# Optimization experiments

Measured on AMD Instinct MI355X. Metric: run time of the kernel, lower is better.

The kernel has to match this reference:

```python
import jax, jax.numpy as jnp
import numpy as np

N, DIN, C, E = 50000, 256, 8, 1600000
N_STEPS = 5


def setup_inputs() -> dict:
    key = jax.random.key(0)
    k1, k2, k3, k4 = jax.random.split(key, 4)
    x = jax.random.normal(k1, (N, DIN), dtype=jnp.float32)
    W = jax.random.normal(k2, (DIN, C), dtype=jnp.float32) / np.float32(np.sqrt(DIN))
    b = jnp.zeros((C,), dtype=jnp.float32)
    edge_index = jax.random.randint(k3, (2, E), 0, N, dtype=jnp.int64)
    rv = jax.random.randint(k4, (E,), 0, E, dtype=jnp.int64)
    return {"x": x, "W": W, "b": b, "edge_index": edge_index, "rv": rv}


def _log_normalize(lx):
    return lx - jax.scipy.special.logsumexp(lx, axis=-1, keepdims=True)


def reference(x, W, b, edge_index, rv):
    # transform: Linear (num_hidden=0) + LogSoftmax -> initial log beliefs
    log_b0 = jax.nn.log_softmax(x @ W + b, axis=-1)            # [N, C]
    src, dst = edge_index[0], edge_index[1]
    n_nodes, n_cls = log_b0.shape
    # learn_coupling=False: log_H = -3 * (ones - eye)
    logH = -3.0 * (jnp.ones((n_cls, n_cls), jnp.float32) - jnp.eye(n_cls, dtype=jnp.float32))
    log_msg = jnp.full((edge_index.shape[1], n_cls), -np.log(n_cls), dtype=jnp.float32)
    log_b = log_b0
    for _ in range(N_STEPS):
        x_j = log_b[src]                                        # [E, C] gather
        t = x_j - log_msg[rv]                                   # [E, C]
        # per-edge logsumexp over incoming class dim against coupling matrix
        raw = jax.scipy.special.logsumexp(t[:, :, None] + logH[None, :, :], axis=1)  # [E, C]
        log_msg = _log_normalize(raw)
        agg = jax.ops.segment_sum(log_msg, dst, num_segments=n_nodes)  # scatter-add
        log_b = _log_normalize(agg + log_b0)
    return log_b
```

## Files before the change

kernel.cpp:

```cpp
#include <hip/hip_runtime.h>

static constexpr int kN   = 50000;
static constexpr int kDin = 256;
static constexpr int kC   = 8;
static constexpr int kE   = 1600000;
static constexpr int kSteps = 5;

static constexpr int kNB      = 256;
static constexpr int kBucketW = 196;
static constexpr int kChunk   = 4096;
static constexpr int kEperB   = kE / kNB;

static constexpr size_t OFF_LOGB0 = 0;
static constexpr size_t OFF_BHIST = 1600000;
static constexpr size_t OFF_GBASE = 1601024;
static constexpr size_t OFF_GCUR  = 1602112;
static constexpr size_t OFF_START = 1603200;
static constexpr size_t OFF_REC   = 1803264;
static constexpr size_t OFF_PAY   = 8203264;
static constexpr size_t OFF_INV   = 21003264;
static constexpr size_t OFF_MSGA  = 27403264;
static constexpr size_t OFF_MSGB  = 40203264;
static constexpr size_t OFF_SPOS  = 53003264;
static constexpr size_t OFF_SRCS  = 59403264;
static constexpr size_t OFF_RVT   = 62603264;
static constexpr size_t OFF_RVS   = 69003264;
static constexpr size_t OFF_REC2  = 75403264;
static constexpr size_t OFF_GCUR2 = 88203264;
static constexpr size_t WS_NEEDED = 88204288;

static constexpr float kDEC8  = 3.0f / 255.0f;
static constexpr float kENC8  = 255.0f / 3.0f;
static constexpr float kOFF   = 3.2990003f;
static constexpr float kA     = 0.049787068367863944f;
static constexpr float kOneMA = 0.950212931632136f;

__global__ void __launch_bounds__(256) init_kernel(
    const float* __restrict__ x, const float* __restrict__ W,
    const float* __restrict__ bias,
    float* __restrict__ log_b0, float* __restrict__ log_b,
    const int* __restrict__ dst, int* __restrict__ bhist)
{
    __shared__ int h[kNB];
    if (blockIdx.x >= 1024) {
        h[threadIdx.x] = 0;
        __syncthreads();
        const int nthr = 256 * 256;
        for (int e = (blockIdx.x - 1024) * 256 + threadIdx.x; e < kE; e += nthr)
            atomicAdd(&h[dst[e] / kBucketW], 1);
        __syncthreads();
        if (h[threadIdx.x]) atomicAdd(&bhist[threadIdx.x], h[threadIdx.x]);
        return;
    }

    const int lane   = threadIdx.x & 63;
    const int wave   = (blockIdx.x * 256 + threadIdx.x) >> 6;
    const int nwaves = (1024 * 256) >> 6;

    float w[4][8];
#pragma unroll
    for (int j = 0; j < 4; ++j) {
        const float4* wp = reinterpret_cast<const float4*>(W + (size_t)(lane + 64 * j) * kC);
        float4 a = wp[0], b2 = wp[1];
        w[j][0] = a.x;  w[j][1] = a.y;  w[j][2] = a.z;  w[j][3] = a.w;
        w[j][4] = b2.x; w[j][5] = b2.y; w[j][6] = b2.z; w[j][7] = b2.w;
    }

    for (int row = wave; row < kN; row += nwaves) {
        const float* xr = x + (size_t)row * kDin;
        float acc[8] = {0.f, 0.f, 0.f, 0.f, 0.f, 0.f, 0.f, 0.f};
#pragma unroll
        for (int j = 0; j < 4; ++j) {
            float xv = xr[lane + 64 * j];
#pragma unroll
            for (int c = 0; c < 8; ++c) acc[c] = fmaf(xv, w[j][c], acc[c]);
        }
#pragma unroll
        for (int off = 32; off > 0; off >>= 1) {
#pragma unroll
            for (int c = 0; c < 8; ++c) acc[c] += __shfl_down(acc[c], off, 64);
        }
        if (lane == 0) {
            float z[8], m = -1e30f;
#pragma unroll
            for (int c = 0; c < 8; ++c) { z[c] = acc[c] + bias[c]; m = fmaxf(m, z[c]); }
            float s = 0.f;
#pragma unroll
            for (int c = 0; c < 8; ++c) s += __expf(z[c] - m);
            float lse = m + __logf(s);
#pragma unroll
            for (int c = 0; c < 8; ++c) {
                float v = z[c] - lse;
                log_b0[(size_t)row * 8 + c] = v;
                log_b[(size_t)row * 8 + c]  = v;
            }
        }
    }
}

__global__ void __launch_bounds__(256) bucket_scan_kernel(
    const int* __restrict__ bhist, int* __restrict__ gbase, int* __restrict__ gcur,
    int* __restrict__ gcur2)
{
    __shared__ int sh[kNB];
    const int tid = threadIdx.x;
    int v = bhist[tid];
    sh[tid] = v;
    __syncthreads();
#pragma unroll
    for (int off = 1; off < kNB; off <<= 1) {
        int t = (tid >= off) ? sh[tid - off] : 0;
        __syncthreads();
        sh[tid] += t;
        __syncthreads();
    }
    int excl = sh[tid] - v;
    gbase[tid] = excl;
    gcur[tid]  = excl;
    gcur2[tid] = tid * kEperB;
    if (tid == kNB - 1) { gbase[kNB] = sh[tid]; gcur[kNB] = sh[tid]; }
}

__global__ void __launch_bounds__(256) bin_kernel(
    const int* __restrict__ dst, const int* __restrict__ src,
    const int* __restrict__ rv, int* __restrict__ gcur,
    unsigned int* __restrict__ recbuf, unsigned long long* __restrict__ paybuf)
{
    __shared__ int hist[kNB];
    __shared__ int sh[kNB];
    __shared__ int cursor[kNB];
    __shared__ int gdbase[kNB];
    __shared__ unsigned int buf[kChunk];
    __shared__ unsigned long long pbuf[kChunk];

    const int tid = threadIdx.x;
    const int e0  = blockIdx.x * kChunk;
    const int n   = (kE - e0 < kChunk) ? (kE - e0) : kChunk;

    hist[tid] = 0;
    __syncthreads();

    int myb[16];
    unsigned int rec[16];
    unsigned long long pay[16];
#pragma unroll
    for (int k = 0; k < 16; ++k) {
        const int i = tid + k * 256;
        myb[k] = -1;
        if (i < n) {
            const int d = dst[e0 + i];
            const int b = d / kBucketW;
            myb[k] = b;
            rec[k] = ((unsigned int)(d - b * kBucketW) << 21) | (unsigned int)(e0 + i);
            pay[k] = ((unsigned long long)(unsigned int)src[e0 + i] << 21)
                   | (unsigned int)rv[e0 + i];
            atomicAdd(&hist[b], 1);
        }
    }
    __syncthreads();

    const int cnt = hist[tid];
    sh[tid] = cnt;
    __syncthreads();
#pragma unroll
    for (int off = 1; off < kNB; off <<= 1) {
        int t = (tid >= off) ? sh[tid - off] : 0;
        __syncthreads();
        sh[tid] += t;
        __syncthreads();
    }
    const int excl = sh[tid] - cnt;
    cursor[tid] = excl;
    __syncthreads();

#pragma unroll
    for (int k = 0; k < 16; ++k) {
        if (myb[k] >= 0) {
            int slot = atomicAdd(&cursor[myb[k]], 1);
            buf[slot]  = rec[k];
            pbuf[slot] = pay[k];
        }
    }
    gdbase[tid] = (cnt > 0) ? atomicAdd(&gcur[tid], cnt) : 0;
    __syncthreads();

    for (int i = tid; i < n; i += 256) {
        int b = 0;
#pragma unroll
        for (int step = 128; step >= 1; step >>= 1)
            if (b + step <= kNB - 1 && sh[b + step - 1] <= i) b += step;
        const int off_in_b = i - (sh[b] - hist[b]);
        recbuf[gdbase[b] + off_in_b] = buf[i];
        paybuf[gdbase[b] + off_in_b] = pbuf[i];
    }
}

__global__ void __launch_bounds__(256) fine_kernel(
    const int* __restrict__ gbase, const unsigned int* __restrict__ recbuf,
    const unsigned long long* __restrict__ paybuf,
    int* __restrict__ start, int* __restrict__ inv,
    unsigned short* __restrict__ src_s, int* __restrict__ rvt)
{
    __shared__ int hist[kNB];
    __shared__ int sh[kNB];
    __shared__ int lcur[kNB];

    const int tid = threadIdx.x;
    const int b   = blockIdx.x;
    const int nb0 = b * kBucketW;
    const int nnode = (kN - nb0 < kBucketW) ? (kN - nb0) : kBucketW;
    const int rb = gbase[b], re = gbase[b + 1];

    hist[tid] = 0;
    __syncthreads();

    for (int i = rb + tid; i < re; i += 256)
        atomicAdd(&hist[recbuf[i] >> 21], 1);
    __syncthreads();

    const int cnt = hist[tid];
    sh[tid] = cnt;
    __syncthreads();
#pragma unroll
    for (int off = 1; off < kNB; off <<= 1) {
        int t = (tid >= off) ? sh[tid - off] : 0;
        __syncthreads();
        sh[tid] += t;
        __syncthreads();
    }
    const int excl = sh[tid] - cnt;
    lcur[tid] = rb + excl;
    if (tid < nnode) start[nb0 + tid] = rb + excl;
    if (b == gridDim.x - 1 && tid == 0) start[kN] = kE;
    __syncthreads();

    for (int i = rb + tid; i < re; i += 256) {
        const unsigned int r = recbuf[i];
        const unsigned long long pay = paybuf[i];
        const int p = atomicAdd(&lcur[r >> 21], 1);
        inv[p]   = (int)(r & 0x1FFFFFu);
        src_s[p] = (unsigned short)(pay >> 21);
        rvt[p]   = (int)(pay & 0x1FFFFFu);
    }
}

__global__ void __launch_bounds__(256) bin2_kernel(
    const int* __restrict__ inv, int* __restrict__ gcur2,
    unsigned long long* __restrict__ recbuf2)
{
    __shared__ int hist[kNB];
    __shared__ int sh[kNB];
    __shared__ int cursor[kNB];
    __shared__ int gdbase[kNB];
    __shared__ unsigned long long buf[kChunk];

    const int tid = threadIdx.x;
    const int p0  = blockIdx.x * kChunk;
    const int n   = (kE - p0 < kChunk) ? (kE - p0) : kChunk;

    hist[tid] = 0;
    __syncthreads();

    int myb[16];
    unsigned long long rec[16];
#pragma unroll
    for (int k = 0; k < 16; ++k) {
        const int i = tid + k * 256;
        myb[k] = -1;
        if (i < n) {
            const int e = inv[p0 + i];
            const int b = e / kEperB;
            myb[k] = b;
            rec[k] = ((unsigned long long)(e - b * kEperB) << 32) | (unsigned int)(p0 + i);
            atomicAdd(&hist[b], 1);
        }
    }
    __syncthreads();

    const int cnt = hist[tid];
    sh[tid] = cnt;
    __syncthreads();
#pragma unroll
    for (int off = 1; off < kNB; off <<= 1) {
        int t = (tid >= off) ? sh[tid - off] : 0;
        __syncthreads();
        sh[tid] += t;
        __syncthreads();
    }
    const int excl = sh[tid] - cnt;
    cursor[tid] = excl;
    __syncthreads();

#pragma unroll
    for (int k = 0; k < 16; ++k) {
        if (myb[k] >= 0) {
            int slot = atomicAdd(&cursor[myb[k]], 1);
            buf[slot] = rec[k];
        }
    }
    gdbase[tid] = (cnt > 0) ? atomicAdd(&gcur2[tid], cnt) : 0;
    __syncthreads();

    for (int i = tid; i < n; i += 256) {
        int b = 0;
#pragma unroll
        for (int step = 128; step >= 1; step >>= 1)
            if (b + step <= kNB - 1 && sh[b + step - 1] <= i) b += step;
        const int off_in_b = i - (sh[b] - hist[b]);
        recbuf2[gdbase[b] + off_in_b] = buf[i];
    }
}

__global__ void __launch_bounds__(256) fine2_kernel(
    const unsigned long long* __restrict__ recbuf2, int* __restrict__ spos)
{
    __shared__ int slot[kEperB];
    const int tid  = threadIdx.x;
    const int base = blockIdx.x * kEperB;

    for (int i = tid; i < kEperB; i += 256) {
        const unsigned long long r = recbuf2[base + i];
        slot[(int)(r >> 32)] = (int)(r & 0xFFFFFFFFu);
    }
    __syncthreads();
    for (int i = tid; i < kEperB; i += 256)
        spos[base + i] = slot[i];
}

__global__ void __launch_bounds__(256) build_kernel(
    const int* __restrict__ rvt, const int* __restrict__ spos,
    int* __restrict__ rv_s)
{
    const int p0 = (blockIdx.x * 256 + threadIdx.x) * 2;
    if (p0 >= kE) return;
    const int2 rr = *reinterpret_cast<const int2*>(rvt + p0);
    *reinterpret_cast<int2*>(rv_s + p0) = make_int2(spos[rr.x], spos[rr.y]);
}

template <bool FIRST>
__device__ inline uint2 proc_edge(float4 l0, float4 l1, uint2 m)
{
    float t[8] = {l0.x, l0.y, l0.z, l0.w, l1.x, l1.y, l1.z, l1.w};
    if (!FIRST) {
        t[0] -= (float)(m.x & 0xffu)         * kDEC8;
        t[1] -= (float)((m.x >> 8) & 0xffu)  * kDEC8;
        t[2] -= (float)((m.x >> 16) & 0xffu) * kDEC8;
        t[3] -= (float)(m.x >> 24)           * kDEC8;
        t[4] -= (float)(m.y & 0xffu)         * kDEC8;
        t[5] -= (float)((m.y >> 8) & 0xffu)  * kDEC8;
        t[6] -= (float)((m.y >> 16) & 0xffu) * kDEC8;
        t[7] -= (float)(m.y >> 24)           * kDEC8;
    }
    float mx = t[0];
#pragma unroll
    for (int c = 1; c < 8; ++c) mx = fmaxf(mx, t[c]);
    float p[8], S = 0.f;
#pragma unroll
    for (int c = 0; c < 8; ++c) { p[c] = __expf(t[c] - mx); S += p[c]; }
    const float coef = kOneMA / S;
    unsigned int q[8];
#pragma unroll
    for (int c = 0; c < 8; ++c) {
        float u  = fmaf(coef, p[c], kA);
        float qq = fmaf(__logf(u), kENC8, 255.0f);
        qq = fminf(fmaxf(qq + 0.5f, 0.0f), 255.0f);
        q[c] = (unsigned int)qq;
    }
    return make_uint2(q[0] | (q[1] << 8) | (q[2] << 16) | (q[3] << 24),
                      q[4] | (q[5] << 8) | (q[6] << 16) | (q[7] << 24));
}

template <bool FIRST>
__global__ void __launch_bounds__(256) edge_kernel(
    const unsigned short* __restrict__ src_s, const int* __restrict__ rv_s,
    const float* __restrict__ log_b,
    const unsigned char* __restrict__ mold,
    unsigned char* __restrict__ mnew)
{
    const int i0 = (blockIdx.x * 256 + threadIdx.x) * 4;
    if (i0 >= kE) return;

    const ushort4 sp = *reinterpret_cast<const ushort4*>(src_s + i0);

    const float4* pa = reinterpret_cast<const float4*>(log_b + (size_t)sp.x * 8);
    const float4* pb = reinterpret_cast<const float4*>(log_b + (size_t)sp.y * 8);
    const float4* pc = reinterpret_cast<const float4*>(log_b + (size_t)sp.z * 8);
    const float4* pd = reinterpret_cast<const float4*>(log_b + (size_t)sp.w * 8);
    float4 a0 = pa[0], a1 = pa[1];
    float4 b0 = pb[0], b1 = pb[1];
    float4 c0 = pc[0], c1 = pc[1];
    float4 d0 = pd[0], d1 = pd[1];

    uint2 m0 = make_uint2(0, 0), m1 = m0, m2 = m0, m3 = m0;
    if (!FIRST) {
        const int4 rp = *reinterpret_cast<const int4*>(rv_s + i0);
        m0 = *reinterpret_cast<const uint2*>(mold + (size_t)rp.x * 8);
        m1 = *reinterpret_cast<const uint2*>(mold + (size_t)rp.y * 8);
        m2 = *reinterpret_cast<const uint2*>(mold + (size_t)rp.z * 8);
        m3 = *reinterpret_cast<const uint2*>(mold + (size_t)rp.w * 8);
    }

    const uint2 o0 = proc_edge<FIRST>(a0, a1, m0);
    const uint2 o1 = proc_edge<FIRST>(b0, b1, m1);
    const uint2 o2 = proc_edge<FIRST>(c0, c1, m2);
    const uint2 o3 = proc_edge<FIRST>(d0, d1, m3);

    uint4* mn = reinterpret_cast<uint4*>(mnew + (size_t)i0 * 8);
    mn[0] = make_uint4(o0.x, o0.y, o1.x, o1.y);
    mn[1] = make_uint4(o2.x, o2.y, o3.x, o3.y);
}

template <bool FINAL>
__global__ void __launch_bounds__(256) node_kernel(
    const int* __restrict__ start,
    const unsigned char* __restrict__ msgq,
    const float* __restrict__ log_b0, float* __restrict__ log_b)
{
    const int wid  = (blockIdx.x * 256 + threadIdx.x) >> 6;
    const int lane = threadIdx.x & 63;
    const int half = lane >> 5;
    const int l32  = lane & 31;
    const int n = wid * 2 + half;
    if (n >= kN) return;

    const int s = start[n], e2 = start[n + 1];

    int q[8] = {0, 0, 0, 0, 0, 0, 0, 0};
    for (int j = s + l32; j < e2; j += 32) {
        const uint2 m = *reinterpret_cast<const uint2*>(msgq + (size_t)j * 8);
        q[0] += (int)(m.x & 0xffu);          q[1] += (int)((m.x >> 8) & 0xffu);
        q[2] += (int)((m.x >> 16) & 0xffu);  q[3] += (int)(m.x >> 24);
        q[4] += (int)(m.y & 0xffu);          q[5] += (int)((m.y >> 8) & 0xffu);
        q[6] += (int)((m.y >> 16) & 0xffu);  q[7] += (int)(m.y >> 24);
    }
#pragma unroll
    for (int off = 1; off <= 16; off <<= 1) {
#pragma unroll
        for (int c = 0; c < 8; ++c) q[c] += __shfl_xor(q[c], off, 64);
    }

    if (l32 == 0) {
        const int deg = e2 - s;
        const float base = -kOFF * (float)deg;
        const float4* lb0 = reinterpret_cast<const float4*>(log_b0 + (size_t)n * 8);
        float4 c0 = lb0[0], c1 = lb0[1];
        float v[8];
        v[0] = fmaf((float)q[0], kDEC8, base) + c0.x;
        v[1] = fmaf((float)q[1], kDEC8, base) + c0.y;
        v[2] = fmaf((float)q[2], kDEC8, base) + c0.z;
        v[3] = fmaf((float)q[3], kDEC8, base) + c0.w;
        v[4] = fmaf((float)q[4], kDEC8, base) + c1.x;
        v[5] = fmaf((float)q[5], kDEC8, base) + c1.y;
        v[6] = fmaf((float)q[6], kDEC8, base) + c1.z;
        v[7] = fmaf((float)q[7], kDEC8, base) + c1.w;
        if (FINAL) {
            float m = v[0];
#pragma unroll
            for (int c = 1; c < 8; ++c) m = fmaxf(m, v[c]);
            float sum = 0.f;
#pragma unroll
            for (int c = 0; c < 8; ++c) sum += __expf(v[c] - m);
            float lse = m + __logf(sum);
#pragma unroll
            for (int c = 0; c < 8; ++c) v[c] -= lse;
        }
        float4* lb = reinterpret_cast<float4*>(log_b + (size_t)n * 8);
        lb[0] = make_float4(v[0], v[1], v[2], v[3]);
        lb[1] = make_float4(v[4], v[5], v[6], v[7]);
    }
}

extern "C" void kernel_launch(void* const* d_in, const int* in_sizes, int n_in,
                              void* d_out, int out_size, void* d_ws, size_t ws_size,
                              hipStream_t stream) {
    const float* x    = (const float*)d_in[0];
    const float* W    = (const float*)d_in[1];
    const float* bias = (const float*)d_in[2];
    const int*   ei   = (const int*)d_in[3];
    const int*   rv   = (const int*)d_in[4];
    const int* src = ei;
    const int* dst = ei + kE;
    float* out = (float*)d_out;

    if (ws_size < WS_NEEDED) return;

    char* ws = (char*)d_ws;
    float* log_b0 = (float*)(ws + OFF_LOGB0);
    int*   bhist  = (int*)(ws + OFF_BHIST);
    int*   gbase  = (int*)(ws + OFF_GBASE);
    int*   gcur   = (int*)(ws + OFF_GCUR);
    int*   start  = (int*)(ws + OFF_START);
    unsigned int*       recbuf = (unsigned int*)(ws + OFF_REC);
    unsigned long long* paybuf = (unsigned long long*)(ws + OFF_PAY);
    int*   inv    = (int*)(ws + OFF_INV);
    unsigned char* msgA = (unsigned char*)(ws + OFF_MSGA);
    unsigned char* msgB = (unsigned char*)(ws + OFF_MSGB);
    int*   spos   = (int*)(ws + OFF_SPOS);
    unsigned short* src_s = (unsigned short*)(ws + OFF_SRCS);
    int*   rvt    = (int*)(ws + OFF_RVT);
    int*   rv_s   = (int*)(ws + OFF_RVS);
    unsigned long long* recbuf2 = (unsigned long long*)(ws + OFF_REC2);
    int*   gcur2  = (int*)(ws + OFF_GCUR2);

    const int edgeBlocks  = (kE / 4 + 255) / 256;
    const int buildBlocks = (kE / 2 + 255) / 256;
    const int nodeBlocks  = ((kN + 1) / 2 * 64 + 255) / 256;
    const int binBlocks   = (kE + kChunk - 1) / kChunk;

    (void)hipMemsetAsync(bhist, 0, kNB * sizeof(int), stream);
    init_kernel<<<1280, 256, 0, stream>>>(x, W, bias, log_b0, out, dst, bhist);
    bucket_scan_kernel<<<1, 256, 0, stream>>>(bhist, gbase, gcur, gcur2);
    bin_kernel<<<binBlocks, 256, 0, stream>>>(dst, src, rv, gcur, recbuf, paybuf);
    fine_kernel<<<kNB, 256, 0, stream>>>(gbase, recbuf, paybuf, start, inv, src_s, rvt);
    bin2_kernel<<<binBlocks, 256, 0, stream>>>(inv, gcur2, recbuf2);
    fine2_kernel<<<kNB, 256, 0, stream>>>(recbuf2, spos);
    build_kernel<<<buildBlocks, 256, 0, stream>>>(rvt, spos, rv_s);

    edge_kernel<true><<<edgeBlocks, 256, 0, stream>>>(src_s, rv_s, out, msgB, msgA);
    node_kernel<false><<<nodeBlocks, 256, 0, stream>>>(start, msgA, log_b0, out);

    unsigned char* cur = msgA;
    unsigned char* nxt = msgB;
    for (int it = 1; it < kSteps; ++it) {
        edge_kernel<false><<<edgeBlocks, 256, 0, stream>>>(src_s, rv_s, out, cur, nxt);
        if (it == kSteps - 1)
            node_kernel<true><<<nodeBlocks, 256, 0, stream>>>(start, nxt, log_b0, out);
        else
            node_kernel<false><<<nodeBlocks, 256, 0, stream>>>(start, nxt, log_b0, out);
        unsigned char* tmp = cur; cur = nxt; nxt = tmp;
    }
}
```

Before: 453.4 us.

## Fuse edge message and node aggregation into one step kernel with LDS reduction

Merges the per-step edge kernel and node kernel into a single step kernel. Each block processes a contiguous dst-sorted range of edges, accumulates quantized messages in LDS per destination node, and writes node beliefs directly. Nodes that span block boundaries are finished through global atomics plus a completion counter. Beliefs ping-pong between two workspace buffers, and the final step skips writing messages. This removes the separate node pass and its re-read of the message array, at the cost of LDS atomics, a per-edge dst array, and cross-block atomic coordination.

```diff
diff --git a/kernel.cpp b/kernel.cpp
--- a/kernel.cpp
+++ b/kernel.cpp
@@ -10,6 +10,7 @@
 static constexpr int kBucketW = 196;
 static constexpr int kChunk   = 4096;
 static constexpr int kEperB   = kE / kNB;
+static constexpr int kEpB     = 1024;
 
 static constexpr size_t OFF_LOGB0 = 0;
 static constexpr size_t OFF_BHIST = 1600000;
@@ -27,7 +28,12 @@
 static constexpr size_t OFF_RVS   = 69003264;
 static constexpr size_t OFF_REC2  = 75403264;
 static constexpr size_t OFF_GCUR2 = 88203264;
-static constexpr size_t WS_NEEDED = 88204288;
+static constexpr size_t OFF_DNODE = 88204288;
+static constexpr size_t OFF_AGG   = 91404288;
+static constexpr size_t OFF_CNT   = 93004288;
+static constexpr size_t OFF_LBA   = 93204288;
+static constexpr size_t OFF_LBB   = 94804288;
+static constexpr size_t WS_NEEDED = 96404288;
 
 static constexpr float kDEC8  = 3.0f / 255.0f;
 static constexpr float kENC8  = 255.0f / 3.0f;
@@ -38,7 +44,8 @@
 __global__ void __launch_bounds__(256) init_kernel(
     const float* __restrict__ x, const float* __restrict__ W,
     const float* __restrict__ bias,
-    float* __restrict__ log_b0, float* __restrict__ log_b,
+    float* __restrict__ log_b0, float* __restrict__ lbA,
+    float* __restrict__ lbB, float* __restrict__ outb,
     const int* __restrict__ dst, int* __restrict__ bhist)
 {
     __shared__ int h[kNB];
@@ -92,7 +99,9 @@
             for (int c = 0; c < 8; ++c) {
                 float v = z[c] - lse;
                 log_b0[(size_t)row * 8 + c] = v;
-                log_b[(size_t)row * 8 + c]  = v;
+                lbA[(size_t)row * 8 + c]    = v;
+                lbB[(size_t)row * 8 + c]    = v;
+                outb[(size_t)row * 8 + c]   = v;
             }
         }
     }
@@ -199,7 +208,8 @@
     const int* __restrict__ gbase, const unsigned int* __restrict__ recbuf,
     const unsigned long long* __restrict__ paybuf,
     int* __restrict__ start, int* __restrict__ inv,
-    unsigned short* __restrict__ src_s, int* __restrict__ rvt)
+    unsigned short* __restrict__ src_s, int* __restrict__ rvt,
+    unsigned short* __restrict__ dnode)
 {
     __shared__ int hist[kNB];
     __shared__ int sh[kNB];
@@ -237,10 +247,12 @@
     for (int i = rb + tid; i < re; i += 256) {
         const unsigned int r = recbuf[i];
         const unsigned long long pay = paybuf[i];
-        const int p = atomicAdd(&lcur[r >> 21], 1);
+        const int local = (int)(r >> 21);
+        const int p = atomicAdd(&lcur[local], 1);
         inv[p]   = (int)(r & 0x1FFFFFu);
         src_s[p] = (unsigned short)(pay >> 21);
         rvt[p]   = (int)(pay & 0x1FFFFFu);
+        dnode[p] = (unsigned short)(nb0 + local);
     }
 }
 
@@ -338,7 +350,7 @@
 }
 
 template <bool FIRST>
-__device__ inline uint2 proc_edge(float4 l0, float4 l1, uint2 m)
+__device__ inline void proc_edge_q(float4 l0, float4 l1, uint2 m, unsigned int q[8])
 {
     float t[8] = {l0.x, l0.y, l0.z, l0.w, l1.x, l1.y, l1.z, l1.w};
     if (!FIRST) {
@@ -358,7 +370,6 @@
 #pragma unroll
     for (int c = 0; c < 8; ++c) { p[c] = __expf(t[c] - mx); S += p[c]; }
     const float coef = kOneMA / S;
-    unsigned int q[8];
 #pragma unroll
     for (int c = 0; c < 8; ++c) {
         float u  = fmaf(coef, p[c], kA);
@@ -366,107 +377,151 @@
         qq = fminf(fmaxf(qq + 0.5f, 0.0f), 255.0f);
         q[c] = (unsigned int)qq;
     }
-    return make_uint2(q[0] | (q[1] << 8) | (q[2] << 16) | (q[3] << 24),
-                      q[4] | (q[5] << 8) | (q[6] << 16) | (q[7] << 24));
-}
-
-template <bool FIRST>
-__global__ void __launch_bounds__(256) edge_kernel(
+}
+
+__device__ inline void node_write(float* __restrict__ lb_write,
+                                  const float* __restrict__ log_b0,
+                                  int n, const int q[8], int deg, bool finalstep)
+{
+    const float base = -kOFF * (float)deg;
+    const float4* lb0 = reinterpret_cast<const float4*>(log_b0 + (size_t)n * 8);
+    float4 c0 = lb0[0], c1 = lb0[1];
+    float v[8];
+    v[0] = fmaf((float)q[0], kDEC8, base) + c0.x;
+    v[1] = fmaf((float)q[1], kDEC8, base) + c0.y;
+    v[2] = fmaf((float)q[2], kDEC8, base) + c0.z;
+    v[3] = fmaf((float)q[3], kDEC8, base) + c0.w;
+    v[4] = fmaf((float)q[4], kDEC8, base) + c1.x;
+    v[5] = fmaf((float)q[5], kDEC8, base) + c1.y;
+    v[6] = fmaf((float)q[6], kDEC8, base) + c1.z;
+    v[7] = fmaf((float)q[7], kDEC8, base) + c1.w;
+    if (finalstep) {
+        float m = v[0];
+#pragma unroll
+        for (int c = 1; c < 8; ++c) m = fmaxf(m, v[c]);
+        float sum = 0.f;
+#pragma unroll
+        for (int c = 0; c < 8; ++c) sum += __expf(v[c] - m);
+        float lse = m + __logf(sum);
+#pragma unroll
+        for (int c = 0; c < 8; ++c) v[c] -= lse;
+    }
+    float4* lb = reinterpret_cast<float4*>(lb_write + (size_t)n * 8);
+    lb[0] = make_float4(v[0], v[1], v[2], v[3]);
+    lb[1] = make_float4(v[4], v[5], v[6], v[7]);
+}
+
+template <bool FIRST, bool FINAL>
+__global__ void __launch_bounds__(256) step_kernel(
     const unsigned short* __restrict__ src_s, const int* __restrict__ rv_s,
-    const float* __restrict__ log_b,
-    const unsigned char* __restrict__ mold,
-    unsigned char* __restrict__ mnew)
-{
-    const int i0 = (blockIdx.x * 256 + threadIdx.x) * 4;
-    if (i0 >= kE) return;
-
-    const ushort4 sp = *reinterpret_cast<const ushort4*>(src_s + i0);
-
-    const float4* pa = reinterpret_cast<const float4*>(log_b + (size_t)sp.x * 8);
-    const float4* pb = reinterpret_cast<const float4*>(log_b + (size_t)sp.y * 8);
-    const float4* pc = reinterpret_cast<const float4*>(log_b + (size_t)sp.z * 8);
-    const float4* pd = reinterpret_cast<const float4*>(log_b + (size_t)sp.w * 8);
-    float4 a0 = pa[0], a1 = pa[1];
-    float4 b0 = pb[0], b1 = pb[1];
-    float4 c0 = pc[0], c1 = pc[1];
-    float4 d0 = pd[0], d1 = pd[1];
-
-    uint2 m0 = make_uint2(0, 0), m1 = m0, m2 = m0, m3 = m0;
-    if (!FIRST) {
-        const int4 rp = *reinterpret_cast<const int4*>(rv_s + i0);
-        m0 = *reinterpret_cast<const uint2*>(mold + (size_t)rp.x * 8);
-        m1 = *reinterpret_cast<const uint2*>(mold + (size_t)rp.y * 8);
-        m2 = *reinterpret_cast<const uint2*>(mold + (size_t)rp.z * 8);
-        m3 = *reinterpret_cast<const uint2*>(mold + (size_t)rp.w * 8);
-    }
-
-    const uint2 o0 = proc_edge<FIRST>(a0, a1, m0);
-    const uint2 o1 = proc_edge<FIRST>(b0, b1, m1);
-    const uint2 o2 = proc_edge<FIRST>(c0, c1, m2);
-    const uint2 o3 = proc_edge<FIRST>(d0, d1, m3);
-
-    uint4* mn = reinterpret_cast<uint4*>(mnew + (size_t)i0 * 8);
-    mn[0] = make_uint4(o0.x, o0.y, o1.x, o1.y);
-    mn[1] = make_uint4(o2.x, o2.y, o3.x, o3.y);
-}
-
-template <bool FINAL>
-__global__ void __launch_bounds__(256) node_kernel(
-    const int* __restrict__ start,
-    const unsigned char* __restrict__ msgq,
-    const float* __restrict__ log_b0, float* __restrict__ log_b)
-{
-    const int wid  = (blockIdx.x * 256 + threadIdx.x) >> 6;
-    const int lane = threadIdx.x & 63;
-    const int half = lane >> 5;
-    const int l32  = lane & 31;
-    const int n = wid * 2 + half;
-    if (n >= kN) return;
-
-    const int s = start[n], e2 = start[n + 1];
-
-    int q[8] = {0, 0, 0, 0, 0, 0, 0, 0};
-    for (int j = s + l32; j < e2; j += 32) {
-        const uint2 m = *reinterpret_cast<const uint2*>(msgq + (size_t)j * 8);
-        q[0] += (int)(m.x & 0xffu);          q[1] += (int)((m.x >> 8) & 0xffu);
-        q[2] += (int)((m.x >> 16) & 0xffu);  q[3] += (int)(m.x >> 24);
-        q[4] += (int)(m.y & 0xffu);          q[5] += (int)((m.y >> 8) & 0xffu);
-        q[6] += (int)((m.y >> 16) & 0xffu);  q[7] += (int)(m.y >> 24);
-    }
-#pragma unroll
-    for (int off = 1; off <= 16; off <<= 1) {
-#pragma unroll
-        for (int c = 0; c < 8; ++c) q[c] += __shfl_xor(q[c], off, 64);
-    }
-
-    if (l32 == 0) {
+    const unsigned short* __restrict__ dnode, const int* __restrict__ start,
+    const float* __restrict__ log_b0,
+    const unsigned char* __restrict__ mold, unsigned char* __restrict__ mnew,
+    int* __restrict__ agg, int* __restrict__ cnt,
+    const float* __restrict__ lb_read, float* __restrict__ lb_write)
+{
+    __shared__ int lds_q[(kEpB + 1) * 8];
+    __shared__ int sh_info[2];
+
+    const int tid = threadIdx.x;
+    const int p0 = blockIdx.x * kEpB;
+    const int p1 = (p0 + kEpB < kE) ? (p0 + kEpB) : kE;
+
+    if (tid == 0) {
+        sh_info[0] = dnode[p0];
+        sh_info[1] = dnode[p1 - 1];
+    }
+    __syncthreads();
+    const int nfirst = sh_info[0];
+    const int nlast  = sh_info[1];
+    const int nspan  = nlast - nfirst + 1;
+
+    for (int i = tid; i < nspan * 8; i += 256) lds_q[i] = 0;
+    __syncthreads();
+
+    const int i0 = p0 + tid * 4;
+    if (i0 < kE) {
+        const ushort4 sp = *reinterpret_cast<const ushort4*>(src_s + i0);
+        const ushort4 dn = *reinterpret_cast<const ushort4*>(dnode + i0);
+
+        const float4* pa = reinterpret_cast<const float4*>(lb_read + (size_t)sp.x * 8);
+        const float4* pb = reinterpret_cast<const float4*>(lb_read + (size_t)sp.y * 8);
+        const float4* pc = reinterpret_cast<const float4*>(lb_read + (size_t)sp.z * 8);
+        const float4* pd = reinterpret_cast<const float4*>(lb_read + (size_t)sp.w * 8);
+        float4 a0 = pa[0], a1 = pa[1];
+        float4 b0 = pb[0], b1 = pb[1];
+        float4 c0 = pc[0], c1 = pc[1];
+        float4 d0 = pd[0], d1 = pd[1];
+
+        uint2 m0 = make_uint2(0, 0), m1 = m0, m2 = m0, m3 = m0;
+        if (!FIRST) {
+            const int4 rp = *reinterpret_cast<const int4*>(rv_s + i0);
+            m0 = *reinterpret_cast<const uint2*>(mold + (size_t)rp.x * 8);
+            m1 = *reinterpret_cast<const uint2*>(mold + (size_t)rp.y * 8);
+            m2 = *reinterpret_cast<const uint2*>(mold + (size_t)rp.z * 8);
+            m3 = *reinterpret_cast<const uint2*>(mold + (size_t)rp.w * 8);
+        }
+
+        unsigned int qa[8], qb[8], qc[8], qd[8];
+        proc_edge_q<FIRST>(a0, a1, m0, qa);
+        proc_edge_q<FIRST>(b0, b1, m1, qb);
+        proc_edge_q<FIRST>(c0, c1, m2, qc);
+        proc_edge_q<FIRST>(d0, d1, m3, qd);
+
+        if (!FINAL) {
+            uint4* mn = reinterpret_cast<uint4*>(mnew + (size_t)i0 * 8);
+            mn[0] = make_uint4(qa[0] | (qa[1] << 8) | (qa[2] << 16) | (qa[3] << 24),
+                               qa[4] | (qa[5] << 8) | (qa[6] << 16) | (qa[7] << 24),
+                               qb[0] | (qb[1] << 8) | (qb[2] << 16) | (qb[3] << 24),
+                               qb[4] | (qb[5] << 8) | (qb[6] << 16) | (qb[7] << 24));
+            mn[1] = make_uint4(qc[0] | (qc[1] << 8) | (qc[2] << 16) | (qc[3] << 24),
+                               qc[4] | (qc[5] << 8) | (qc[6] << 16) | (qc[7] << 24),
+                               qd[0] | (qd[1] << 8) | (qd[2] << 16) | (qd[3] << 24),
+                               qd[4] | (qd[5] << 8) | (qd[6] << 16) | (qd[7] << 24));
+        }
+
+        int ba = ((int)dn.x - nfirst) * 8;
+        int bb = ((int)dn.y - nfirst) * 8;
+        int bc = ((int)dn.z - nfirst) * 8;
+        int bd = ((int)dn.w - nfirst) * 8;
+#pragma unroll
+        for (int c = 0; c < 8; ++c) atomicAdd(&lds_q[ba + c], (int)qa[c]);
+#pragma unroll
+        for (int c = 0; c < 8; ++c) atomicAdd(&lds_q[bb + c], (int)qb[c]);
+#pragma unroll
+        for (int c = 0; c < 8; ++c) atomicAdd(&lds_q[bc + c], (int)qc[c]);
+#pragma unroll
+        for (int c = 0; c < 8; ++c) atomicAdd(&lds_q[bd + c], (int)qd[c]);
+    }
+    __syncthreads();
+
+    for (int n = nfirst + tid; n <= nlast; n += 256) {
+        const int s  = start[n];
+        const int e2 = start[n + 1];
         const int deg = e2 - s;
-        const float base = -kOFF * (float)deg;
-        const float4* lb0 = reinterpret_cast<const float4*>(log_b0 + (size_t)n * 8);
-        float4 c0 = lb0[0], c1 = lb0[1];
-        float v[8];
-        v[0] = fmaf((float)q[0], kDEC8, base) + c0.x;
-        v[1] = fmaf((float)q[1], kDEC8, base) + c0.y;
-        v[2] = fmaf((float)q[2], kDEC8, base) + c0.z;
-        v[3] = fmaf((float)q[3], kDEC8, base) + c0.w;
-        v[4] = fmaf((float)q[4], kDEC8, base) + c1.x;
-        v[5] = fmaf((float)q[5], kDEC8, base) + c1.y;
-        v[6] = fmaf((float)q[6], kDEC8, base) + c1.z;
-        v[7] = fmaf((float)q[7], kDEC8, base) + c1.w;
-        if (FINAL) {
-            float m = v[0];
-#pragma unroll
-            for (int c = 1; c < 8; ++c) m = fmaxf(m, v[c]);
-            float sum = 0.f;
-#pragma unroll
-            for (int c = 0; c < 8; ++c) sum += __expf(v[c] - m);
-            float lse = m + __logf(sum);
-#pragma unroll
-            for (int c = 0; c < 8; ++c) v[c] -= lse;
-        }
-        float4* lb = reinterpret_cast<float4*>(log_b + (size_t)n * 8);
-        lb[0] = make_float4(v[0], v[1], v[2], v[3]);
-        lb[1] = make_float4(v[4], v[5], v[6], v[7]);
+        const int base = (n - nfirst) * 8;
+        if (s >= p0 && e2 <= p1) {
+            int q[8];
+#pragma unroll
+            for (int c = 0; c < 8; ++c) q[c] = lds_q[base + c];
+            node_write(lb_write, log_b0, n, q, deg, FINAL);
+        } else {
+            const int lo = (s > p0) ? s : p0;
+            const int hi = (e2 < p1) ? e2 : p1;
+            const int my = hi - lo;
+#pragma unroll
+            for (int c = 0; c < 8; ++c) atomicAdd(&agg[(size_t)n * 8 + c], lds_q[base + c]);
+            __threadfence();
+            const int old = atomicAdd(&cnt[n], my);
+            if (old + my == deg) {
+                __threadfence();
+                int q[8];
+#pragma unroll
+                for (int c = 0; c < 8; ++c) q[c] = atomicExch(&agg[(size_t)n * 8 + c], 0);
+                atomicSub(&cnt[n], deg);
+                node_write(lb_write, log_b0, n, q, deg, FINAL);
+            }
+        }
     }
 }
 
@@ -501,32 +556,29 @@
     int*   rv_s   = (int*)(ws + OFF_RVS);
     unsigned long long* recbuf2 = (unsigned long long*)(ws + OFF_REC2);
     int*   gcur2  = (int*)(ws + OFF_GCUR2);
-
-    const int edgeBlocks  = (kE / 4 + 255) / 256;
+    unsigned short* dnode = (unsigned short*)(ws + OFF_DNODE);
+    int*   agg    = (int*)(ws + OFF_AGG);
+    int*   cnt    = (int*)(ws + OFF_CNT);
+    float* lbA    = (float*)(ws + OFF_LBA);
+    float* lbB    = (float*)(ws + OFF_LBB);
+
+    const int stepBlocks  = (kE + kEpB - 1) / kEpB;
     const int buildBlocks = (kE / 2 + 255) / 256;
-    const int nodeBlocks  = ((kN + 1) / 2 * 64 + 255) / 256;
     const int binBlocks   = (kE + kChunk - 1) / kChunk;
 
     (void)hipMemsetAsync(bhist, 0, kNB * sizeof(int), stream);
-    init_kernel<<<1280, 256, 0, stream>>>(x, W, bias, log_b0, out, dst, bhist);
+    (void)hipMemsetAsync(agg, 0, (size_t)kN * 8 * sizeof(int) + (size_t)kN * sizeof(int), stream);
+    init_kernel<<<1280, 256, 0, stream>>>(x, W, bias, log_b0, lbA, lbB, out, dst, bhist);
     bucket_scan_kernel<<<1, 256, 0, stream>>>(bhist, gbase, gcur, gcur2);
     bin_kernel<<<binBlocks, 256, 0, stream>>>(dst, src, rv, gcur, recbuf, paybuf);
-    fine_kernel<<<kNB, 256, 0, stream>>>(gbase, recbuf, paybuf, start, inv, src_s, rvt);
+    fine_kernel<<<kNB, 256, 0, stream>>>(gbase, recbuf, paybuf, start, inv, src_s, rvt, dnode);
     bin2_kernel<<<binBlocks, 256, 0, stream>>>(inv, gcur2, recbuf2);
     fine2_kernel<<<kNB, 256, 0, stream>>>(recbuf2, spos);
     build_kernel<<<buildBlocks, 256, 0, stream>>>(rvt, spos, rv_s);
 
-    edge_kernel<true><<<edgeBlocks, 256, 0, stream>>>(src_s, rv_s, out, msgB, msgA);
-    node_kernel<false><<<nodeBlocks, 256, 0, stream>>>(start, msgA, log_b0, out);
-
-    unsigned char* cur = msgA;
-    unsigned char* nxt = msgB;
-    for (int it = 1; it < kSteps; ++it) {
-        edge_kernel<false><<<edgeBlocks, 256, 0, stream>>>(src_s, rv_s, out, cur, nxt);
-        if (it == kSteps - 1)
-            node_kernel<true><<<nodeBlocks, 256, 0, stream>>>(start, nxt, log_b0, out);
-        else
-            node_kernel<false><<<nodeBlocks, 256, 0, stream>>>(start, nxt, log_b0, out);
-        unsigned char* tmp = cur; cur = nxt; nxt = tmp;
-    }
-}
+    step_kernel<true,  false><<<stepBlocks, 256, 0, stream>>>(src_s, rv_s, dnode, start, log_b0, msgB, msgA, agg, cnt, lbA, lbB);
+    step_kernel<false, false><<<stepBlocks, 256, 0, stream>>>(src_s, rv_s, dnode, start, log_b0, msgA, msgB, agg, cnt, lbB, lbA);
+    step_kernel<false, false><<<stepBlocks, 256, 0, stream>>>(src_s, rv_s, dnode, start, log_b0, msgB, msgA, agg, cnt, lbA, lbB);
+    step_kernel<false, false><<<stepBlocks, 256, 0, stream>>>(src_s, rv_s, dnode, start, log_b0, msgA, msgB, agg, cnt, lbB, lbA);
+    step_kernel<false, true ><<<stepBlocks, 256, 0, stream>>>(src_s, rv_s, dnode, start, log_b0, msgB, msgA, agg, cnt, lbA, out);
+}
```

New measurement: 904.5 us. +99.5%, slower.
